# Kernel optimization log

Measured on AMD Instinct MI355X. Metric: run time of the kernel, lower is better.

Reference implementation:

```python
import jax, jax.numpy as jnp
import numpy as np
import math

B, L, D_MODEL, D_K, H = 2, 1024, 1024, 1024, 16
HD = D_K // H  # 64, even
EPS = 1e-5


def setup_inputs() -> dict:
    key = jax.random.key(0)
    ks = jax.random.split(key, 16)
    s = 0.02
    inp = {
        'word_embed': jax.random.normal(ks[0], (B, L, D_MODEL), jnp.float32),
        'speaker_embed': jax.random.normal(ks[1], (B, L, D_MODEL), jnp.float32),
        'mask': jnp.broadcast_to(jnp.tril(jnp.ones((L, L), jnp.int32)), (B, L, L)),
        'qw_w': jax.random.normal(ks[2], (D_K, D_MODEL), jnp.float32) * s,
        'qw_b': jnp.zeros((D_K,), jnp.float32),
        'kw_w': jax.random.normal(ks[3], (D_K, D_MODEL), jnp.float32) * s,
        'kw_b': jnp.zeros((D_K,), jnp.float32),
        'qs_w': jax.random.normal(ks[4], (D_K, D_MODEL), jnp.float32) * s,
        'qs_b': jnp.zeros((D_K,), jnp.float32),
        'ks_w': jax.random.normal(ks[5], (D_K, D_MODEL), jnp.float32) * s,
        'ks_b': jnp.zeros((D_K,), jnp.float32),
        'v_w': jax.random.normal(ks[6], (D_K, D_MODEL), jnp.float32) * s,
        'v_b': jnp.zeros((D_K,), jnp.float32),
        'out_w': jax.random.normal(ks[7], (D_MODEL, D_K), jnp.float32) * s,
        'out_b': jnp.zeros((D_MODEL,), jnp.float32),
        'gamma': jnp.ones((HD,), jnp.float32),
        'beta': jnp.zeros((HD,), jnp.float32),
    }
    return inp


def _rotary_tables(seq_len, dim, dtype):
    pos = jnp.arange(seq_len, dtype=dtype)[:, None]  # [L,1]
    div = jnp.exp(jnp.arange(0, dim, 2, dtype=dtype) * (-math.log(10000.0) / dim))
    return jnp.sin(pos * div), jnp.cos(pos * div)  # each [L, dim//2]


def _rotary(x, sin, cos):
    # x: [B,H,L,HD]; NOTE: original concatenates halves (non-interleaved output)
    x1, x2 = x[..., 0::2], x[..., 1::2]
    return jnp.concatenate([x1 * cos - x2 * sin, x1 * sin + x2 * cos], axis=-1)


def _layernorm(x, gamma, beta):
    mu = jnp.mean(x, axis=-1, keepdims=True)
    var = jnp.mean(jnp.square(x - mu), axis=-1, keepdims=True)
    return (x - mu) * jax.lax.rsqrt(var + EPS) * gamma + beta


def _split(x):
    b, l, _ = x.shape
    return x.reshape(b, l, H, HD).transpose(0, 2, 1, 3)  # [B,H,L,HD]


def reference(word_embed, speaker_embed, mask, qw_w, qw_b, kw_w, kw_b,
              qs_w, qs_b, ks_w, ks_b, v_w, v_b, out_w, out_b, gamma, beta):
    proj = lambda x, w, b: jnp.einsum('bld,kd->blk', x, w) + b
    qw = _split(proj(word_embed, qw_w, qw_b))
    kw = _split(proj(word_embed, kw_w, kw_b))
    qs = _split(proj(speaker_embed, qs_w, qs_b))
    ks = _split(proj(speaker_embed, ks_w, ks_b))
    v = _split(proj(word_embed, v_w, v_b))

    sin, cos = _rotary_tables(word_embed.shape[1], HD, word_embed.dtype)
    ln = lambda x: _layernorm(_rotary(x, sin, cos), gamma, beta)
    qw, kw, qs, ks = ln(qw), ln(kw), ln(qs), ln(ks)

    scores = (jnp.einsum('bhqd,bhkd->bhqk', qw, kw)
              + jnp.einsum('bhqd,bhkd->bhqk', qs, ks)) / math.sqrt(2 * HD)
    scores = jnp.where(mask[:, None] == 0, -jnp.inf, scores)
    attn = jax.nn.softmax(scores, axis=-1)  # dropout is eval-mode no-op
    out = jnp.einsum('bhqk,bhkd->bhqd', attn, v)
    out = out.transpose(0, 2, 1, 3).reshape(out.shape[0], out.shape[2], D_K)
    out = jnp.einsum('blk,dk->bld', out, out_w) + out_b
    return (out, attn)
```

## Files before the change

### kernel.cpp

```cpp
#include <hip/hip_runtime.h>
#include <cstdint>
#include <cstddef>

typedef __bf16 bf16x8 __attribute__((ext_vector_type(8)));
typedef float  f32x4  __attribute__((ext_vector_type(4)));
typedef unsigned short ushort8_t __attribute__((ext_vector_type(8)));

__device__ __forceinline__ unsigned short f2bf(float f){
  unsigned u = __builtin_bit_cast(unsigned, f);
  u += 0x7fffu + ((u >> 16) & 1u);
  return (unsigned short)(u >> 16);
}
__device__ __forceinline__ float bf2f(unsigned short s){
  return __builtin_bit_cast(float, ((unsigned)s) << 16);
}

#define MFMA16(a,b,c) __builtin_amdgcn_mfma_f32_16x16x32_bf16((a),(b),(c),0,0,0)

__device__ __forceinline__ void gload16(const void* g, void* lds){
  __builtin_amdgcn_global_load_lds(
      (const __attribute__((address_space(1))) void*)g,
      (__attribute__((address_space(3))) void*)lds, 16, 0, 0);
}

#define E_XW    ((size_t)0)
#define E_XS    (E_XW    + (size_t)2048*1024)
#define E_WWORD (E_XS    + (size_t)2048*1024)
#define E_WSPK  (E_WWORD + (size_t)3072*1024)
#define E_WOUT  (E_WSPK  + (size_t)2048*1024)
#define E_PWORD (E_WOUT  + (size_t)1024*1024)
#define E_PSPK  (E_PWORD + (size_t)2048*3072)
#define E_VT    (E_PSPK  + (size_t)2048*2048)
#define E_CTX   (E_VT    + (size_t)2048*1024)
#define E_END   (E_CTX   + (size_t)2048*1024)

__global__ __launch_bounds__(256) void convert_all(
    const float* __restrict__ word, const float* __restrict__ spk,
    const float* __restrict__ qww,  const float* __restrict__ kww,
    const float* __restrict__ vw,   const float* __restrict__ qsw,
    const float* __restrict__ ksw,  const float* __restrict__ outw,
    const float* __restrict__ qwb,  const float* __restrict__ kwb,
    const float* __restrict__ vb,   const float* __restrict__ qsb,
    const float* __restrict__ ksb,
    unsigned short* __restrict__ wsb, float* __restrict__ FB)
{
  int idx = blockIdx.x*256 + threadIdx.x;
  if (idx < 32768){
    int pos = idx >> 5, i = idx & 31;
    float inv = expf((float)(2*i) * -0.14391157f);
    float ang = (float)pos * inv;
    float sv, cv; sincosf(ang, &sv, &cv);
    FB[5120 + idx]         = sv;
    FB[5120 + 32768 + idx] = cv;
  } else if (idx < 33792){
    int i = idx - 32768;
    FB[i] = qwb[i]; FB[1024+i] = kwb[i]; FB[2048+i] = vb[i];
    FB[3072+i] = qsb[i]; FB[3072+1024+i] = ksb[i];
  }

  const size_t total = 2621440;
  for (size_t c = (size_t)blockIdx.x*256 + threadIdx.x; c < total;
       c += (size_t)gridDim.x*256){
    const float* src; size_t dst; size_t i;
    if (c < 524288)       { src = word; dst = E_XW; i = c; }
    else if (c < 1048576) { src = spk;  dst = E_XS; i = c - 524288; }
    else {
      size_t t = c - 1048576; int seg = (int)(t >> 18); i = t & 262143;
      switch (seg){
        case 0:  src = qww; dst = E_WWORD;                      break;
        case 1:  src = kww; dst = E_WWORD + (size_t)1048576;    break;
        case 2:  src = vw;  dst = E_WWORD + (size_t)2097152;    break;
        case 3:  src = qsw; dst = E_WSPK;                       break;
        case 4:  src = ksw; dst = E_WSPK  + (size_t)1048576;    break;
        default: src = outw; dst = E_WOUT;                      break;
      }
    }
    float4 v = ((const float4*)src)[i];
    ushort4 o; o.x = f2bf(v.x); o.y = f2bf(v.y); o.z = f2bf(v.z); o.w = f2bf(v.w);
    ((ushort4*)(wsb + dst))[i] = o;
  }
}

template<int NF>
__device__ __forceinline__ void gemm_body(
    const unsigned short* __restrict__ A, const unsigned short* __restrict__ Bw,
    const float* __restrict__ bias, void* __restrict__ Cv,
    int N, int K, int bid, int out_bf16,
    unsigned short* As, unsigned short* Bs)
{
  const int BN = NF*32;
  const int nbn = N / BN;
  const int bm = bid / nbn, bn = bid % nbn;
  const int tid = threadIdx.x;
  const int l = tid & 63, w = tid >> 6;
  const int wm = w >> 1, wn = w & 1;
  const int li = l & 15, lg = l >> 4;

  f32x4 acc[4][NF];
  #pragma unroll
  for (int a = 0; a < 4; a++)
    #pragma unroll
    for (int b = 0; b < NF; b++) acc[a][b] = (f32x4){0.f,0.f,0.f,0.f};

  const int colS = (l & 3) * 8;
  const size_t aBase = (size_t)(bm*128) * K;
  const size_t bBase = (size_t)(bn*BN) * K;

  for (int kt = 0; kt < K; kt += 32){
    #pragma unroll
    for (int j = 0; j < 2; j++){
      int row = (w*2 + j)*16 + (l >> 2);
      gload16(A + aBase + (size_t)row*K + kt + colS, &As[(size_t)(w*2+j)*512]);
    }
    if (NF == 4){
      #pragma unroll
      for (int j = 0; j < 2; j++){
        int row = (w*2 + j)*16 + (l >> 2);
        gload16(Bw + bBase + (size_t)row*K + kt + colS, &Bs[(size_t)(w*2+j)*512]);
      }
    } else {
      int row = w*16 + (l >> 2);
      gload16(Bw + bBase + (size_t)row*K + kt + colS, &Bs[(size_t)w*512]);
    }
    asm volatile("s_waitcnt vmcnt(0)" ::: "memory");
    __syncthreads();

    bf16x8 af[4], bfr[NF];
    const int ko = lg * 8;
    #pragma unroll
    for (int fm = 0; fm < 4; fm++)
      af[fm] = *(const bf16x8*)&As[(wm*64 + fm*16 + li)*32 + ko];
    #pragma unroll
    for (int fn = 0; fn < NF; fn++)
      bfr[fn] = *(const bf16x8*)&Bs[(wn*(NF*16) + fn*16 + li)*32 + ko];
    #pragma unroll
    for (int fm = 0; fm < 4; fm++)
      #pragma unroll
      for (int fn = 0; fn < NF; fn++)
        acc[fm][fn] = MFMA16(af[fm], bfr[fn], acc[fm][fn]);
    __syncthreads();
  }

  #pragma unroll
  for (int fm = 0; fm < 4; fm++){
    int m0 = bm*128 + wm*64 + fm*16 + lg*4;
    #pragma unroll
    for (int fn = 0; fn < NF; fn++){
      int n = bn*BN + wn*(NF*16) + fn*16 + li;
      float bv = bias ? bias[n] : 0.f;
      #pragma unroll
      for (int r = 0; r < 4; r++){
        float v = acc[fm][fn][r] + bv;
        if (out_bf16) ((unsigned short*)Cv)[(size_t)(m0+r)*N + n] = f2bf(v);
        else          ((float*)Cv)[(size_t)(m0+r)*N + n] = v;
      }
    }
  }
}

__global__ __launch_bounds__(256) void gemm_qkv(
    const unsigned short* __restrict__ XW, const unsigned short* __restrict__ WWORD,
    const unsigned short* __restrict__ XS, const unsigned short* __restrict__ WSPK,
    const float* __restrict__ FB,
    unsigned short* __restrict__ PWORD, unsigned short* __restrict__ PSPK)
{
  __shared__ unsigned short As[128*32];
  __shared__ unsigned short Bs[128*32];
  int bid = blockIdx.x;
  if (bid < 384)
    gemm_body<4>(XW, WWORD, FB,        PWORD, 3072, 1024, bid,       1, As, Bs);
  else
    gemm_body<4>(XS, WSPK,  FB + 3072, PSPK,  2048, 1024, bid - 384, 1, As, Bs);
}

__global__ __launch_bounds__(256) void gemm_out(
    const unsigned short* __restrict__ CTX, const unsigned short* __restrict__ WOUT,
    const float* __restrict__ outb, float* __restrict__ outp)
{
  __shared__ unsigned short As[128*32];
  __shared__ unsigned short Bs[64*32];
  gemm_body<2>(CTX, WOUT, outb, outp, 1024, 1024, blockIdx.x, 0, As, Bs);
}

__global__ __launch_bounds__(256) void postproc(
    unsigned short* __restrict__ Pw, unsigned short* __restrict__ Ps,
    const float* __restrict__ gamma, const float* __restrict__ beta,
    const float* __restrict__ TS, const float* __restrict__ TC,
    unsigned short* __restrict__ VT)
{
  __shared__ float lds[2320];
  int bx = blockIdx.x;
  int t = threadIdx.x;
  if (bx < 4096){
    int sec = bx & 3, rp = bx >> 2;
    int half = t >> 7, c = t & 127;
    int row = rp*2 + half;
    int seg = c >> 3, j = c & 7;
    unsigned short* p;
    if      (sec == 0) p = Pw + (size_t)row*3072 +        seg*64;
    else if (sec == 1) p = Pw + (size_t)row*3072 + 1024 + seg*64;
    else if (sec == 2) p = Ps + (size_t)row*2048 +        seg*64;
    else               p = Ps + (size_t)row*2048 + 1024 + seg*64;
    int pos = row & 1023;
    int sl  = half*16 + seg;

    ushort8_t xv = *(const ushort8_t*)(p + j*8);
    float4 sv = *(const float4*)&TS[pos*32 + j*4];
    float4 cv = *(const float4*)&TC[pos*32 + j*4];
    float ss[4] = {sv.x, sv.y, sv.z, sv.w};
    float cc[4] = {cv.x, cv.y, cv.z, cv.w};
    float y1[4], y2[4];
    #pragma unroll
    for (int k = 0; k < 4; k++){
      float x0 = bf2f(xv[2*k]), x1 = bf2f(xv[2*k+1]);
      y1[k] = x0*cc[k] - x1*ss[k];
      y2[k] = x0*ss[k] + x1*cc[k];
    }
    *(float4*)&lds[sl*68 + j*4]      = (float4){y1[0], y1[1], y1[2], y1[3]};
    *(float4*)&lds[sl*68 + 32 + j*4] = (float4){y2[0], y2[1], y2[2], y2[3]};
    __syncthreads();

    float4 a0 = *(const float4*)&lds[sl*68 + j*8];
    float4 a1 = *(const float4*)&lds[sl*68 + j*8 + 4];
    float v[8] = {a0.x, a0.y, a0.z, a0.w, a1.x, a1.y, a1.z, a1.w};
    float s = 0.f;
    #pragma unroll
    for (int k = 0; k < 8; k++) s += v[k];
    #pragma unroll
    for (int o = 1; o < 8; o <<= 1) s += __shfl_xor(s, o);
    float mu = s * (1.f/64.f);
    float sq = 0.f;
    #pragma unroll
    for (int k = 0; k < 8; k++){ float d = v[k] - mu; sq += d*d; }
    #pragma unroll
    for (int o = 1; o < 8; o <<= 1) sq += __shfl_xor(sq, o);
    float rs = rsqrtf(sq * (1.f/64.f) + 1e-5f);
    float4 g0 = *(const float4*)&gamma[j*8], g1 = *(const float4*)&gamma[j*8+4];
    float4 b0 = *(const float4*)&beta[j*8],  b1 = *(const float4*)&beta[j*8+4];
    float gg[8] = {g0.x,g0.y,g0.z,g0.w,g1.x,g1.y,g1.z,g1.w};
    float bb[8] = {b0.x,b0.y,b0.z,b0.w,b1.x,b1.y,b1.z,b1.w};
    ushort8_t o8;
    #pragma unroll
    for (int k = 0; k < 8; k++) o8[k] = f2bf((v[k]-mu)*rs*gg[k] + bb[k]);
    *(ushort8_t*)(p + j*8) = o8;
  } else {
    unsigned short* tp = (unsigned short*)lds;
    int bid2 = bx - 4096;
    int bh = bid2 >> 4, lt = bid2 & 15;
    int b = bh >> 4, h = bh & 15;
    #pragma unroll
    for (int i = 0; i < 2; i++){
      int cc2 = t + i*256;
      int row = cc2 >> 3, co = (cc2 & 7)*8;
      const unsigned short* src = Pw + (size_t)(b*1024 + lt*64 + row)*3072 + 2048 + h*64 + co;
      *(uint4*)&tp[row*72 + co] = *(const uint4*)src;
    }
    __syncthreads();
    int d = t >> 2, jb = (t & 3)*16;
    unsigned short o[16];
    #pragma unroll
    for (int j = 0; j < 16; j++) o[j] = tp[(jb + j)*72 + d];
    unsigned short* dst = VT + ((size_t)bh*64 + d)*1024 + lt*64 + jb;
    *(uint4*)dst       = *(uint4*)&o[0];
    *(uint4*)(dst + 8) = *(uint4*)&o[8];
  }
}

__global__ __launch_bounds__(512) void attn_fused(
    const unsigned short* __restrict__ Pw, const unsigned short* __restrict__ Ps,
    const unsigned short* __restrict__ VTg,
    float* __restrict__ attn, unsigned short* __restrict__ Ctx)
{
  __shared__ unsigned short SL[36864];

  int bx = blockIdx.x;
  int b = bx >> 7, rem = bx & 127, h = rem >> 3, qq = rem & 7;
  int maxkt = 15 - qq;
  int tid = threadIdx.x;
  int w = tid >> 6, l = tid & 63;
  int g = w >> 2, wsub = w & 3;
  int qt = g ? maxkt : qq;
  int lg = l >> 4, li = l & 15;
  int q0 = qt*64 + wsub*16;
  int bh = b*16 + h;

  int srow = tid >> 3, scb = tid & 7;
  const unsigned short* gKW = Pw + (size_t)(b*1024)*3072 + 1024 + h*64;
  const unsigned short* gKS = Ps + (size_t)(b*1024)*2048 + 1024 + h*64;
  const unsigned short* gVT = VTg + (size_t)bh*64*1024;
  unsigned short* pt = SL + 27648 + w*1152;

  bf16x8 aqw[2], aqs[2];
  {
    int q = q0 + li;
    const unsigned short* pqw = Pw + (size_t)(b*1024 + q)*3072 + h*64 + lg*8;
    const unsigned short* pqs = Ps + (size_t)(b*1024 + q)*2048 + h*64 + lg*8;
    aqw[0] = *(const bf16x8*)pqw;  aqw[1] = *(const bf16x8*)(pqw + 32);
    aqs[0] = *(const bf16x8*)pqs;  aqs[1] = *(const bf16x8*)(pqs + 32);
  }
  const float rscale = 0.08838834764831845f;

  uint4 rkw, rks, rvt;

  float ps4[4] = {0.f, 0.f, 0.f, 0.f};
  rkw = *(const uint4*)(gKW + (size_t)srow*3072 + scb*8);
  rks = *(const uint4*)(gKS + (size_t)srow*2048 + scb*8);
  *(uint4*)(SL +        srow*72 + scb*8) = rkw;
  *(uint4*)(SL + 9216 + srow*72 + scb*8) = rks;

  for (int kt = 0; kt <= maxkt; ++kt){
    int buf = kt & 1;
    if (kt < maxkt){
      rkw = *(const uint4*)(gKW + (size_t)((kt+1)*64 + srow)*3072 + scb*8);
      rks = *(const uint4*)(gKS + (size_t)((kt+1)*64 + srow)*2048 + scb*8);
    }
    __syncthreads();
    if (kt <= qt){
      const unsigned short* KWt = SL +        buf*4608;
      const unsigned short* KSt = SL + 9216 + buf*4608;
      f32x4 s[4];
      #pragma unroll
      for (int fn = 0; fn < 4; fn++){
        s[fn] = (f32x4){0.f,0.f,0.f,0.f};
        int rr = (fn*16 + li)*72;
        bf16x8 k0 = *(const bf16x8*)(KWt + rr + lg*8);
        bf16x8 k1 = *(const bf16x8*)(KWt + rr + 32 + lg*8);
        bf16x8 k2 = *(const bf16x8*)(KSt + rr + lg*8);
        bf16x8 k3 = *(const bf16x8*)(KSt + rr + 32 + lg*8);
        s[fn] = MFMA16(aqw[0], k0, s[fn]);
        s[fn] = MFMA16(aqw[1], k1, s[fn]);
        s[fn] = MFMA16(aqs[0], k2, s[fn]);
        s[fn] = MFMA16(aqs[1], k3, s[fn]);
      }
      #pragma unroll
      for (int r = 0; r < 4; r++){
        int q = q0 + lg*4 + r;
        #pragma unroll
        for (int fn = 0; fn < 4; fn++){
          int k = kt*64 + fn*16 + li;
          float e = __expf(s[fn][r] * rscale);
          ps4[r] += (k <= q) ? e : 0.f;
        }
      }
    }
    if (kt < maxkt){
      int nb = buf ^ 1;
      *(uint4*)(SL +        nb*4608 + srow*72 + scb*8) = rkw;
      *(uint4*)(SL + 9216 + nb*4608 + srow*72 + scb*8) = rks;
    }
  }
  #pragma unroll
  for (int r = 0; r < 4; r++){
    #pragma unroll
    for (int o = 1; o < 16; o <<= 1) ps4[r] += __shfl_xor(ps4[r], o);
  }
  float rinv[4];
  #pragma unroll
  for (int r = 0; r < 4; r++) rinv[r] = 1.f / ps4[r];

  __syncthreads();
  rkw = *(const uint4*)(gKW + (size_t)srow*3072 + scb*8);
  rks = *(const uint4*)(gKS + (size_t)srow*2048 + scb*8);
  rvt = *(const uint4*)(gVT + (size_t)srow*1024 + scb*8);
  *(uint4*)(SL +         srow*72 + scb*8) = rkw;
  *(uint4*)(SL +  9216 + srow*72 + scb*8) = rks;
  *(uint4*)(SL + 18432 + srow*72 + scb*8) = rvt;

  f32x4 c[4];
  #pragma unroll
  for (int fn = 0; fn < 4; fn++) c[fn] = (f32x4){0.f,0.f,0.f,0.f};

  for (int kt = 0; kt < 16; ++kt){
    int buf = kt & 1;
    if (kt < maxkt){
      rkw = *(const uint4*)(gKW + (size_t)((kt+1)*64 + srow)*3072 + scb*8);
      rks = *(const uint4*)(gKS + (size_t)((kt+1)*64 + srow)*2048 + scb*8);
      rvt = *(const uint4*)(gVT + (size_t)srow*1024 + (kt+1)*64 + scb*8);
    }
    __syncthreads();
    float* abase = attn + ((size_t)bh*1024 + q0 + li)*1024 + kt*64;
    if (kt <= qt){
      const unsigned short* KWt = SL +         buf*4608;
      const unsigned short* KSt = SL +  9216 + buf*4608;
      const unsigned short* VTt = SL + 18432 + buf*4608;
      f32x4 s[4];
      #pragma unroll
      for (int fn = 0; fn < 4; fn++){
        s[fn] = (f32x4){0.f,0.f,0.f,0.f};
        int rr = (fn*16 + li)*72;
        bf16x8 k0 = *(const bf16x8*)(KWt + rr + lg*8);
        bf16x8 k1 = *(const bf16x8*)(KWt + rr + 32 + lg*8);
        bf16x8 k2 = *(const bf16x8*)(KSt + rr + lg*8);
        bf16x8 k3 = *(const bf16x8*)(KSt + rr + 32 + lg*8);
        s[fn] = MFMA16(aqw[0], k0, s[fn]);
        s[fn] = MFMA16(aqw[1], k1, s[fn]);
        s[fn] = MFMA16(aqs[0], k2, s[fn]);
        s[fn] = MFMA16(aqs[1], k3, s[fn]);
      }
      #pragma unroll
      for (int fn = 0; fn < 4; fn++){
        #pragma unroll
        for (int r = 0; r < 4; r++){
          int k = kt*64 + fn*16 + li;
          int q = q0 + lg*4 + r;
          float pp = (k <= q) ? __expf(s[fn][r] * rscale) * rinv[r] : 0.f;
          pt[(lg*4 + r)*72 + fn*16 + li] = f2bf(pp);
        }
      }
      asm volatile("s_waitcnt lgkmcnt(0)" ::: "memory");
      __builtin_amdgcn_sched_barrier(0);
      bf16x8 af0 = *(const bf16x8*)(pt + li*72 + lg*8);
      bf16x8 af1 = *(const bf16x8*)(pt + li*72 + 32 + lg*8);
      ushort8_t u0 = __builtin_bit_cast(ushort8_t, af0);
      ushort8_t u1 = __builtin_bit_cast(ushort8_t, af1);
      *(float4*)(abase + lg*8)          = (float4){bf2f(u0[0]),bf2f(u0[1]),bf2f(u0[2]),bf2f(u0[3])};
      *(float4*)(abase + lg*8 + 4)      = (float4){bf2f(u0[4]),bf2f(u0[5]),bf2f(u0[6]),bf2f(u0[7])};
      *(float4*)(abase + 32 + lg*8)     = (float4){bf2f(u1[0]),bf2f(u1[1]),bf2f(u1[2]),bf2f(u1[3])};
      *(float4*)(abase + 32 + lg*8 + 4) = (float4){bf2f(u1[4]),bf2f(u1[5]),bf2f(u1[6]),bf2f(u1[7])};
      #pragma unroll
      for (int fn = 0; fn < 4; fn++){
        int rr = (fn*16 + li)*72;
        bf16x8 v0 = *(const bf16x8*)(VTt + rr + lg*8);
        bf16x8 v1 = *(const bf16x8*)(VTt + rr + 32 + lg*8);
        c[fn] = MFMA16(af0, v0, c[fn]);
        c[fn] = MFMA16(af1, v1, c[fn]);
      }
    } else {
      float4 z = {0.f, 0.f, 0.f, 0.f};
      *(float4*)(abase + lg*8)          = z;
      *(float4*)(abase + lg*8 + 4)      = z;
      *(float4*)(abase + 32 + lg*8)     = z;
      *(float4*)(abase + 32 + lg*8 + 4) = z;
    }
    if (kt < maxkt){
      int nb = buf ^ 1;
      *(uint4*)(SL +         nb*4608 + srow*72 + scb*8) = rkw;
      *(uint4*)(SL +  9216 + nb*4608 + srow*72 + scb*8) = rks;
      *(uint4*)(SL + 18432 + nb*4608 + srow*72 + scb*8) = rvt;
    }
  }

  #pragma unroll
  for (int fn = 0; fn < 4; fn++){
    #pragma unroll
    for (int r = 0; r < 4; r++){
      int q = q0 + lg*4 + r;
      int d = fn*16 + li;
      Ctx[(size_t)(b*1024 + q)*1024 + h*64 + d] = f2bf(c[fn][r]);
    }
  }
}

extern "C" void kernel_launch(void* const* d_in, const int* in_sizes, int n_in,
                              void* d_out, int out_size, void* d_ws, size_t ws_size,
                              hipStream_t stream)
{
  (void)in_sizes; (void)n_in; (void)out_size; (void)ws_size;
  const float* word = (const float*)d_in[0];
  const float* spk  = (const float*)d_in[1];
  const float* qww  = (const float*)d_in[3];
  const float* qwb  = (const float*)d_in[4];
  const float* kww  = (const float*)d_in[5];
  const float* kwb  = (const float*)d_in[6];
  const float* qsw  = (const float*)d_in[7];
  const float* qsb  = (const float*)d_in[8];
  const float* ksw  = (const float*)d_in[9];
  const float* ksb  = (const float*)d_in[10];
  const float* vw   = (const float*)d_in[11];
  const float* vb   = (const float*)d_in[12];
  const float* outw = (const float*)d_in[13];
  const float* outb = (const float*)d_in[14];
  const float* gamma= (const float*)d_in[15];
  const float* beta = (const float*)d_in[16];

  unsigned short* U = (unsigned short*)d_ws;
  unsigned short* XW    = U + E_XW;
  unsigned short* XS    = U + E_XS;
  unsigned short* WWORD = U + E_WWORD;
  unsigned short* WSPK  = U + E_WSPK;
  unsigned short* WOUT  = U + E_WOUT;
  unsigned short* PWORD = U + E_PWORD;
  unsigned short* PSPK  = U + E_PSPK;
  unsigned short* VT    = U + E_VT;
  unsigned short* CTX   = U + E_CTX;
  float* FB = (float*)(U + E_END);
  float* TS = FB + 5120;
  float* TC = TS + 32768;

  float* outp = (float*)d_out;
  float* attn = outp + (size_t)2*1024*1024;

  convert_all<<<4096, 256, 0, stream>>>(word, spk, qww, kww, vw, qsw, ksw, outw,
                                        qwb, kwb, vb, qsb, ksb, U, FB);
  gemm_qkv<<<640, 256, 0, stream>>>(XW, WWORD, XS, WSPK, FB, PWORD, PSPK);
  postproc<<<4608, 256, 0, stream>>>(PWORD, PSPK, gamma, beta, TS, TC, VT);
  attn_fused<<<256, 512, 0, stream>>>(PWORD, PSPK, VT, attn, CTX);
  gemm_out<<<256, 256, 0, stream>>>(CTX, WOUT, outb, outp);
}
```

Baseline: 120.9 us.

## Double-buffer GEMM LDS tiles and use nontemporal stores for attention probabilities

The shared GEMM body now prefetches the next K-slice of A and B into a second LDS buffer while MFMAs run on the current one, so there is one barrier per iteration instead of two and load latency overlaps compute. K is hardcoded to 1024 and the bias null check is removed. The large fp32 attention-probability writes in the attention kernel become nontemporal stores to reduce cache pollution. LDS use per GEMM block doubles, which may lower occupancy.

```diff
diff --git a/kernel.cpp b/kernel.cpp
--- a/kernel.cpp
+++ b/kernel.cpp
@@ -21,6 +21,10 @@
   __builtin_amdgcn_global_load_lds(
       (const __attribute__((address_space(1))) void*)g,
       (__attribute__((address_space(3))) void*)lds, 16, 0, 0);
+}
+
+__device__ __forceinline__ void nt_store4(float* p, f32x4 v){
+  __builtin_nontemporal_store(v, (f32x4*)p);
 }
 
 #define E_XW    ((size_t)0)
@@ -85,9 +89,10 @@
 __device__ __forceinline__ void gemm_body(
     const unsigned short* __restrict__ A, const unsigned short* __restrict__ Bw,
     const float* __restrict__ bias, void* __restrict__ Cv,
-    int N, int K, int bid, int out_bf16,
+    int N, int bid, int out_bf16,
     unsigned short* As, unsigned short* Bs)
 {
+  const int K = 1024;
   const int BN = NF*32;
   const int nbn = N / BN;
   const int bm = bid / nbn, bn = bid % nbn;
@@ -95,6 +100,8 @@
   const int l = tid & 63, w = tid >> 6;
   const int wm = w >> 1, wn = w & 1;
   const int li = l & 15, lg = l >> 4;
+  const int ABUF = 128*32;
+  const int BBUF = BN*32;
 
   f32x4 acc[4][NF];
   #pragma unroll
@@ -102,43 +109,55 @@
     #pragma unroll
     for (int b = 0; b < NF; b++) acc[a][b] = (f32x4){0.f,0.f,0.f,0.f};
 
-  const int colS = (l & 3) * 8;
   const size_t aBase = (size_t)(bm*128) * K;
   const size_t bBase = (size_t)(bn*BN) * K;
 
+  #pragma unroll
+  for (int j = 0; j < 2; j++){
+    int c = (w*2 + j)*64 + l;
+    gload16(A + aBase + (size_t)(c >> 2)*K + (c & 3)*8, &As[(w*2+j)*512]);
+  }
+  #pragma unroll
+  for (int j = 0; j < NF/2; j++){
+    int c = (w*(NF/2) + j)*64 + l;
+    gload16(Bw + bBase + (size_t)(c >> 2)*K + (c & 3)*8, &Bs[(w*(NF/2)+j)*512]);
+  }
+  asm volatile("s_waitcnt vmcnt(0)" ::: "memory");
+  __syncthreads();
+
+  int cur = 0;
   for (int kt = 0; kt < K; kt += 32){
-    #pragma unroll
-    for (int j = 0; j < 2; j++){
-      int row = (w*2 + j)*16 + (l >> 2);
-      gload16(A + aBase + (size_t)row*K + kt + colS, &As[(size_t)(w*2+j)*512]);
-    }
-    if (NF == 4){
+    if (kt + 32 < K){
+      int nb = cur ^ 1;
       #pragma unroll
       for (int j = 0; j < 2; j++){
-        int row = (w*2 + j)*16 + (l >> 2);
-        gload16(Bw + bBase + (size_t)row*K + kt + colS, &Bs[(size_t)(w*2+j)*512]);
-      }
-    } else {
-      int row = w*16 + (l >> 2);
-      gload16(Bw + bBase + (size_t)row*K + kt + colS, &Bs[(size_t)w*512]);
-    }
+        int c = (w*2 + j)*64 + l;
+        gload16(A + aBase + (size_t)(c >> 2)*K + kt + 32 + (c & 3)*8,
+                &As[nb*ABUF + (w*2+j)*512]);
+      }
+      #pragma unroll
+      for (int j = 0; j < NF/2; j++){
+        int c = (w*(NF/2) + j)*64 + l;
+        gload16(Bw + bBase + (size_t)(c >> 2)*K + kt + 32 + (c & 3)*8,
+                &Bs[nb*BBUF + (w*(NF/2)+j)*512]);
+      }
+    }
+    bf16x8 af[4], bfr[NF];
+    const int ko = lg * 8;
+    #pragma unroll
+    for (int fm = 0; fm < 4; fm++)
+      af[fm] = *(const bf16x8*)&As[cur*ABUF + (wm*64 + fm*16 + li)*32 + ko];
+    #pragma unroll
+    for (int fn = 0; fn < NF; fn++)
+      bfr[fn] = *(const bf16x8*)&Bs[cur*BBUF + (wn*(NF*16) + fn*16 + li)*32 + ko];
+    #pragma unroll
+    for (int fm = 0; fm < 4; fm++)
+      #pragma unroll
+      for (int fn = 0; fn < NF; fn++)
+        acc[fm][fn] = MFMA16(af[fm], bfr[fn], acc[fm][fn]);
     asm volatile("s_waitcnt vmcnt(0)" ::: "memory");
     __syncthreads();
-
-    bf16x8 af[4], bfr[NF];
-    const int ko = lg * 8;
-    #pragma unroll
-    for (int fm = 0; fm < 4; fm++)
-      af[fm] = *(const bf16x8*)&As[(wm*64 + fm*16 + li)*32 + ko];
-    #pragma unroll
-    for (int fn = 0; fn < NF; fn++)
-      bfr[fn] = *(const bf16x8*)&Bs[(wn*(NF*16) + fn*16 + li)*32 + ko];
-    #pragma unroll
-    for (int fm = 0; fm < 4; fm++)
-      #pragma unroll
-      for (int fn = 0; fn < NF; fn++)
-        acc[fm][fn] = MFMA16(af[fm], bfr[fn], acc[fm][fn]);
-    __syncthreads();
+    cur ^= 1;
   }
 
   #pragma unroll
@@ -147,7 +166,7 @@
     #pragma unroll
     for (int fn = 0; fn < NF; fn++){
       int n = bn*BN + wn*(NF*16) + fn*16 + li;
-      float bv = bias ? bias[n] : 0.f;
+      float bv = bias[n];
       #pragma unroll
       for (int r = 0; r < 4; r++){
         float v = acc[fm][fn][r] + bv;
@@ -164,22 +183,22 @@
     const float* __restrict__ FB,
     unsigned short* __restrict__ PWORD, unsigned short* __restrict__ PSPK)
 {
-  __shared__ unsigned short As[128*32];
-  __shared__ unsigned short Bs[128*32];
+  __shared__ unsigned short As[2*128*32];
+  __shared__ unsigned short Bs[2*128*32];
   int bid = blockIdx.x;
   if (bid < 384)
-    gemm_body<4>(XW, WWORD, FB,        PWORD, 3072, 1024, bid,       1, As, Bs);
+    gemm_body<4>(XW, WWORD, FB,        PWORD, 3072, bid,       1, As, Bs);
   else
-    gemm_body<4>(XS, WSPK,  FB + 3072, PSPK,  2048, 1024, bid - 384, 1, As, Bs);
+    gemm_body<4>(XS, WSPK,  FB + 3072, PSPK,  2048, bid - 384, 1, As, Bs);
 }
 
 __global__ __launch_bounds__(256) void gemm_out(
     const unsigned short* __restrict__ CTX, const unsigned short* __restrict__ WOUT,
     const float* __restrict__ outb, float* __restrict__ outp)
 {
-  __shared__ unsigned short As[128*32];
-  __shared__ unsigned short Bs[64*32];
-  gemm_body<2>(CTX, WOUT, outb, outp, 1024, 1024, blockIdx.x, 0, As, Bs);
+  __shared__ unsigned short As[2*128*32];
+  __shared__ unsigned short Bs[2*64*32];
+  gemm_body<2>(CTX, WOUT, outb, outp, 1024, blockIdx.x, 0, As, Bs);
 }
 
 __global__ __launch_bounds__(256) void postproc(
@@ -413,10 +432,14 @@
       bf16x8 af1 = *(const bf16x8*)(pt + li*72 + 32 + lg*8);
       ushort8_t u0 = __builtin_bit_cast(ushort8_t, af0);
       ushort8_t u1 = __builtin_bit_cast(ushort8_t, af1);
-      *(float4*)(abase + lg*8)          = (float4){bf2f(u0[0]),bf2f(u0[1]),bf2f(u0[2]),bf2f(u0[3])};
-      *(float4*)(abase + lg*8 + 4)      = (float4){bf2f(u0[4]),bf2f(u0[5]),bf2f(u0[6]),bf2f(u0[7])};
-      *(float4*)(abase + 32 + lg*8)     = (float4){bf2f(u1[0]),bf2f(u1[1]),bf2f(u1[2]),bf2f(u1[3])};
-      *(float4*)(abase + 32 + lg*8 + 4) = (float4){bf2f(u1[4]),bf2f(u1[5]),bf2f(u1[6]),bf2f(u1[7])};
+      f32x4 w0 = {bf2f(u0[0]),bf2f(u0[1]),bf2f(u0[2]),bf2f(u0[3])};
+      f32x4 w1 = {bf2f(u0[4]),bf2f(u0[5]),bf2f(u0[6]),bf2f(u0[7])};
+      f32x4 w2 = {bf2f(u1[0]),bf2f(u1[1]),bf2f(u1[2]),bf2f(u1[3])};
+      f32x4 w3 = {bf2f(u1[4]),bf2f(u1[5]),bf2f(u1[6]),bf2f(u1[7])};
+      nt_store4(abase + lg*8,          w0);
+      nt_store4(abase + lg*8 + 4,      w1);
+      nt_store4(abase + 32 + lg*8,     w2);
+      nt_store4(abase + 32 + lg*8 + 4, w3);
       #pragma unroll
       for (int fn = 0; fn < 4; fn++){
         int rr = (fn*16 + li)*72;
@@ -426,11 +449,11 @@
         c[fn] = MFMA16(af1, v1, c[fn]);
       }
     } else {
-      float4 z = {0.f, 0.f, 0.f, 0.f};
-      *(float4*)(abase + lg*8)          = z;
-      *(float4*)(abase + lg*8 + 4)      = z;
-      *(float4*)(abase + 32 + lg*8)     = z;
-      *(float4*)(abase + 32 + lg*8 + 4) = z;
+      f32x4 z = {0.f, 0.f, 0.f, 0.f};
+      nt_store4(abase + lg*8,          z);
+      nt_store4(abase + lg*8 + 4,      z);
+      nt_store4(abase + 32 + lg*8,     z);
+      nt_store4(abase + 32 + lg*8 + 4, z);
     }
     if (kt < maxkt){
       int nb = buf ^ 1;
```

Measured after the change: 190.2 us. 1.57x slower.
